# Kernel optimization log

Hardware: AMD Instinct MI355X
Metric: run time of the kernel (lower is better)

## Reference

```python
import jax, jax.numpy as jnp
import numpy as np

EPS = 1e-12  # guard sqrt at zero distance


def setup_inputs() -> dict:
    key = jax.random.key(0)
    k1, k2 = jax.random.split(key)
    B, C, N = 4, 3, 8192
    predict_pc = jax.random.normal(k1, (B, C, N), dtype=jnp.float32)
    gt_pc = jax.random.normal(k2, (B, C, N), dtype=jnp.float32)
    return {"predict_pc": predict_pc, "gt_pc": gt_pc}


def reference(predict_pc, gt_pc):
    # predict_pc: [B, 3, Np], gt_pc: [B, 3, Ng]
    B = gt_pc.shape[0]
    Np = predict_pc.shape[2]
    Ng = gt_pc.shape[2]
    denom = B * (Ng + Np)

    # Pairwise Euclidean distances d[b, n, m] = ||predict[b,:,n] - gt[b,:,m]||
    # via the |p|^2 + |g|^2 - 2 p.g expansion (avoids [B,3,Np,Ng] intermediate).
    p2 = jnp.sum(predict_pc * predict_pc, axis=1)            # [B, Np]
    g2 = jnp.sum(gt_pc * gt_pc, axis=1)                      # [B, Ng]
    dot = jnp.einsum('bcn,bcm->bnm', predict_pc, gt_pc)      # [B, Np, Ng]
    d2 = p2[:, :, None] + g2[:, None, :] - 2.0 * dot         # [B, Np, Ng]
    d = jnp.sqrt(jnp.maximum(d2, EPS))

    # z: for each gt point, distance to nearest predicted point -> min over Np
    z = jnp.min(d, axis=1)   # [B, Ng]
    # z_2: for each predicted point, distance to nearest gt point -> min over Ng
    z2 = jnp.min(d, axis=2)  # [B, Np]

    loss = z.sum() / denom + z2.sum() / denom
    return loss
```

## Files before the change

### kernel.cpp

```cpp
#include <hip/hip_runtime.h>
#include <math.h>


#define B_       4
#define N_       8192
#define THREADS  256
#define RX       16
#define XB       (THREADS * RX)
#define XBLKS    (N_ / XB)
#define YSPLITS  64
#define YCHUNK   (N_ / YSPLITS)
#define NGROUPS  8
#define BLKS_PER_GROUP (XBLKS * YSPLITS)
#define POISON   0xAAAAAAAAu


__global__ __launch_bounds__(THREADS, 4)
void chamfer_fused_kernel(const float* __restrict__ P, const float* __restrict__ G,
                          unsigned* __restrict__ mins, unsigned* __restrict__ gcnt,
                          unsigned* __restrict__ fcnt, float* __restrict__ gsum,
                          float* __restrict__ out)
{
    __shared__ float4 ytile[YCHUNK + 4];
    __shared__ float red[THREADS];
    __shared__ unsigned s_ticket;

    const int t      = threadIdx.x;
    const int xblk   = blockIdx.x;
    const int ysplit = blockIdx.y;
    const int bz     = blockIdx.z;
    const int pass   = bz >> 2;
    const int b      = bz & 3;
    const int grp    = bz;

    const float* Xb = (pass ? G : P) + (size_t)b * 3 * N_;
    const float* Yb = (pass ? P : G) + (size_t)b * 3 * N_;

    if (t < YCHUNK) {
        const int n = ysplit * YCHUNK + t;
        float gx = Yb[n];
        float gy = Yb[N_ + n];
        float gz = Yb[2 * N_ + n];
        ytile[t] = make_float4(gx, gy, gz, fmaf(gx, gx, fmaf(gy, gy, gz * gz)));
    }

    const int xbase = xblk * XB;
    float m2x[RX], m2y[RX], m2z[RX], p2[RX], mn[RX];
#pragma unroll
    for (int i = 0; i < RX; ++i) {
        const int n = xbase + i * THREADS + t;
        float px = Xb[n];
        float py = Xb[N_ + n];
        float pz = Xb[2 * N_ + n];
        p2[i]  = fmaf(px, px, fmaf(py, py, pz * pz));
        m2x[i] = -2.0f * px;
        m2y[i] = -2.0f * py;
        m2z[i] = -2.0f * pz;
        mn[i]  = 3.4e38f;
    }
    __syncthreads();

    float4 g = ytile[0];
#pragma unroll 2
    for (int j = 0; j < YCHUNK; ++j) {
        float4 gn = ytile[j + 1];
#pragma unroll
        for (int i = 0; i < RX; ++i) {
            float s = fmaf(m2x[i], g.x, g.w);
            s = fmaf(m2y[i], g.y, s);
            s = fmaf(m2z[i], g.z, s);
            mn[i] = fminf(mn[i], s);
        }
        g = gn;
    }

    unsigned* mybase = mins + (size_t)grp * N_ + xbase;
#pragma unroll
    for (int i = 0; i < RX; ++i) {
        float v = fmaxf(mn[i] + p2[i], 1e-12f);
        atomicMin(&mybase[i * THREADS + t], __float_as_uint(v));
    }

    __syncthreads();
    if (t == 0) {
        __threadfence();
        s_ticket = atomicAdd(&gcnt[grp], 1u);
    }
    __syncthreads();
    if (s_ticket != POISON + (unsigned)(BLKS_PER_GROUP - 1)) return;

    __threadfence();
    const uint4* v = (const uint4*)(mins + (size_t)grp * N_);
    float acc = 0.0f;
#pragma unroll
    for (int k = 0; k < N_ / 4 / THREADS; ++k) {
        uint4 q = v[k * THREADS + t];
        acc += sqrtf(__uint_as_float(q.x)) + sqrtf(__uint_as_float(q.y))
             + sqrtf(__uint_as_float(q.z)) + sqrtf(__uint_as_float(q.w));
    }
    red[t] = acc;
    __syncthreads();
    for (int off = 128; off > 0; off >>= 1) {
        if (t < off) red[t] += red[t + off];
        __syncthreads();
    }
    if (t == 0) {
        gsum[grp] = red[0];
        __threadfence();
        s_ticket = atomicAdd(fcnt, 1u);
    }
    __syncthreads();
    if (s_ticket != POISON + (unsigned)(NGROUPS - 1)) return;

    __threadfence();
    if (t == 0) {
        float s = 0.0f;
#pragma unroll
        for (int k = 0; k < NGROUPS; ++k) s += gsum[k];
        out[0] = s * (1.0f / 65536.0f);
    }
}

extern "C" void kernel_launch(void* const* d_in, const int* in_sizes, int n_in,
                              void* d_out, int out_size, void* d_ws, size_t ws_size,
                              hipStream_t stream)
{
    const float* P = (const float*)d_in[0];
    const float* G = (const float*)d_in[1];
    float* out = (float*)d_out;

    unsigned* w    = (unsigned*)d_ws;
    unsigned* mins = w;
    unsigned* gcnt = w + 65536;
    unsigned* fcnt = w + 65600;
    float*    gsum = (float*)(w + 65664);

    dim3 grid(XBLKS, YSPLITS, 2 * B_);
    chamfer_fused_kernel<<<grid, THREADS, 0, stream>>>(P, G, mins, gcnt, fcnt, gsum, out);
}
```

Measured before the change: 104.5 us.

## Use packed FP32 FMA over pairs of Y points in the distance loop

The shared Y tile now stores two points per pair of float4 slots in SoA form (x0,x1,y0,y1 / z0,z1,w0,w1). The inner loop uses inline-asm v_pk_fma_f32 with op_sel to evaluate each X point against two Y points in one packed instruction, aiming to halve FMA issue count. The min reduction then uses a chained fminf over both lanes. Inline asm can block compiler scheduling, and the op_sel semantics must be right for the results to be correct.

```diff
diff --git a/kernel.cpp b/kernel.cpp
--- a/kernel.cpp
+++ b/kernel.cpp
@@ -14,6 +14,21 @@
 #define BLKS_PER_GROUP (XBLKS * YSPLITS)
 #define POISON   0xAAAAAAAAu
 
+typedef float v2f __attribute__((ext_vector_type(2)));
+
+__device__ __forceinline__ v2f pk_fma_blo(v2f a, v2f b, v2f c) {
+    v2f d;
+    asm("v_pk_fma_f32 %0, %1, %2, %3 op_sel:[0,0,0] op_sel_hi:[0,1,1]"
+        : "=v"(d) : "v"(a), "v"(b), "v"(c));
+    return d;
+}
+__device__ __forceinline__ v2f pk_fma_bhi(v2f a, v2f b, v2f c) {
+    v2f d;
+    asm("v_pk_fma_f32 %0, %1, %2, %3 op_sel:[1,0,0] op_sel_hi:[1,1,1]"
+        : "=v"(d) : "v"(a), "v"(b), "v"(c));
+    return d;
+}
+
 
 __global__ __launch_bounds__(THREADS, 4)
 void chamfer_fused_kernel(const float* __restrict__ P, const float* __restrict__ G,
@@ -21,7 +36,7 @@
                           unsigned* __restrict__ fcnt, float* __restrict__ gsum,
                           float* __restrict__ out)
 {
-    __shared__ float4 ytile[YCHUNK + 4];
+    __shared__ float4 ytile[2 * (YCHUNK / 2) + 4];
     __shared__ float red[THREADS];
     __shared__ unsigned s_ticket;
 
@@ -36,42 +51,58 @@
     const float* Xb = (pass ? G : P) + (size_t)b * 3 * N_;
     const float* Yb = (pass ? P : G) + (size_t)b * 3 * N_;
 
-    if (t < YCHUNK) {
-        const int n = ysplit * YCHUNK + t;
-        float gx = Yb[n];
-        float gy = Yb[N_ + n];
-        float gz = Yb[2 * N_ + n];
-        ytile[t] = make_float4(gx, gy, gz, fmaf(gx, gx, fmaf(gy, gy, gz * gz)));
+    if (t < YCHUNK / 2) {
+        const int n0 = ysplit * YCHUNK + 2 * t;
+        float2 x01 = *(const float2*)&Yb[n0];
+        float2 y01 = *(const float2*)&Yb[N_ + n0];
+        float2 z01 = *(const float2*)&Yb[2 * N_ + n0];
+        float w0 = fmaf(x01.x, x01.x, fmaf(y01.x, y01.x, z01.x * z01.x));
+        float w1 = fmaf(x01.y, x01.y, fmaf(y01.y, y01.y, z01.y * z01.y));
+        ytile[2 * t]     = make_float4(x01.x, x01.y, y01.x, y01.y);
+        ytile[2 * t + 1] = make_float4(z01.x, z01.y, w0, w1);
     }
 
     const int xbase = xblk * XB;
-    float m2x[RX], m2y[RX], m2z[RX], p2[RX], mn[RX];
+    v2f cm2x[RX / 2], cm2y[RX / 2], cm2z[RX / 2];
+    float p2[RX], mn[RX];
 #pragma unroll
-    for (int i = 0; i < RX; ++i) {
-        const int n = xbase + i * THREADS + t;
-        float px = Xb[n];
-        float py = Xb[N_ + n];
-        float pz = Xb[2 * N_ + n];
-        p2[i]  = fmaf(px, px, fmaf(py, py, pz * pz));
-        m2x[i] = -2.0f * px;
-        m2y[i] = -2.0f * py;
-        m2z[i] = -2.0f * pz;
-        mn[i]  = 3.4e38f;
+    for (int k = 0; k < RX / 2; ++k) {
+        const int n0 = xbase + (2 * k) * THREADS + t;
+        const int n1 = xbase + (2 * k + 1) * THREADS + t;
+        float px0 = Xb[n0], py0 = Xb[N_ + n0], pz0 = Xb[2 * N_ + n0];
+        float px1 = Xb[n1], py1 = Xb[N_ + n1], pz1 = Xb[2 * N_ + n1];
+        p2[2 * k]     = fmaf(px0, px0, fmaf(py0, py0, pz0 * pz0));
+        p2[2 * k + 1] = fmaf(px1, px1, fmaf(py1, py1, pz1 * pz1));
+        cm2x[k] = (v2f){-2.0f * px0, -2.0f * px1};
+        cm2y[k] = (v2f){-2.0f * py0, -2.0f * py1};
+        cm2z[k] = (v2f){-2.0f * pz0, -2.0f * pz1};
+        mn[2 * k] = 3.4e38f;
+        mn[2 * k + 1] = 3.4e38f;
     }
     __syncthreads();
 
-    float4 g = ytile[0];
-#pragma unroll 2
-    for (int j = 0; j < YCHUNK; ++j) {
-        float4 gn = ytile[j + 1];
+    float4 a4 = ytile[0];
+    float4 b4 = ytile[1];
+    for (int jj = 0; jj < YCHUNK / 2; ++jj) {
+        float4 a4n = ytile[2 * jj + 2];
+        float4 b4n = ytile[2 * jj + 3];
+        v2f gx2 = (v2f){a4.x, a4.y};
+        v2f gy2 = (v2f){a4.z, a4.w};
+        v2f gz2 = (v2f){b4.x, b4.y};
+        v2f gw2 = (v2f){b4.z, b4.w};
 #pragma unroll
-        for (int i = 0; i < RX; ++i) {
-            float s = fmaf(m2x[i], g.x, g.w);
-            s = fmaf(m2y[i], g.y, s);
-            s = fmaf(m2z[i], g.z, s);
-            mn[i] = fminf(mn[i], s);
+        for (int k = 0; k < RX / 2; ++k) {
+            v2f s = pk_fma_blo(cm2z[k], gz2, gw2);
+            s = pk_fma_blo(cm2y[k], gy2, s);
+            s = pk_fma_blo(cm2x[k], gx2, s);
+            mn[2 * k] = fminf(fminf(mn[2 * k], s.x), s.y);
+            v2f u = pk_fma_bhi(cm2z[k], gz2, gw2);
+            u = pk_fma_bhi(cm2y[k], gy2, u);
+            u = pk_fma_bhi(cm2x[k], gx2, u);
+            mn[2 * k + 1] = fminf(fminf(mn[2 * k + 1], u.x), u.y);
         }
-        g = gn;
+        a4 = a4n;
+        b4 = b4n;
     }
 
     unsigned* mybase = mins + (size_t)grp * N_ + xbase;
```

New measurement: 104.0 us. About the same (-0.4%).

## Compute pairwise distances with bf16 split-precision MFMA and fuse both min directions

Applied to the files above, without the earlier changes.

Replaces the scalar FMA distance loop with MFMA 16x16x32 bf16 instructions. Each coordinate and squared norm is split into high and low bf16 parts so the dot product keeps near-fp32 accuracy. Both the row minimum and the column minimum now come from one distance tile, which removes the second pass over swapped inputs and halves the pairwise work. Column minima go through shared-memory atomics before the global atomicMin. The risks are the bf16 split losing accuracy for near-zero distances and more atomic contention.

```diff
diff --git a/kernel.cpp b/kernel.cpp
--- a/kernel.cpp
+++ b/kernel.cpp
@@ -2,101 +2,182 @@
 #include <math.h>
 
 
-#define B_       4
-#define N_       8192
-#define THREADS  256
-#define RX       16
-#define XB       (THREADS * RX)
-#define XBLKS    (N_ / XB)
-#define YSPLITS  64
-#define YCHUNK   (N_ / YSPLITS)
-#define NGROUPS  8
-#define BLKS_PER_GROUP (XBLKS * YSPLITS)
-#define POISON   0xAAAAAAAAu
-
-
-__global__ __launch_bounds__(THREADS, 4)
-void chamfer_fused_kernel(const float* __restrict__ P, const float* __restrict__ G,
-                          unsigned* __restrict__ mins, unsigned* __restrict__ gcnt,
-                          unsigned* __restrict__ fcnt, float* __restrict__ gsum,
-                          float* __restrict__ out)
+#define B_        4
+#define N_        8192
+#define THREADS   256
+#define ROWS_PB   256
+#define ROWBLKS   (N_ / ROWS_PB)
+#define MRANGE    1024
+#define MSPLIT    (N_ / MRANGE)
+#define MTILES    (MRANGE / 16)
+#define NGROUPS   B_
+#define BLKS_PER_GROUP (ROWBLKS * MSPLIT)
+#define POISON    0xAAAAAAAAu
+#define INF_BITS  0x7F800000u
+
+typedef __bf16 bf16x8 __attribute__((ext_vector_type(8)));
+typedef float  f32x4  __attribute__((ext_vector_type(4)));
+
+#define SM_ZERO   0
+#define SM_A      16
+#define SM_B      8208
+#define SM_COL    40976
+#define SM_ROW    45072
+#define SM_BYTES  46096
+
+__device__ __forceinline__ unsigned short bf16_rne(float f) {
+    unsigned u = __float_as_uint(f);
+    return (unsigned short)((u + 0x7FFFu + ((u >> 16) & 1u)) >> 16);
+}
+__device__ __forceinline__ float bf16_tof(unsigned short h) {
+    return __uint_as_float(((unsigned)h) << 16);
+}
+
+__device__ __forceinline__ void slotsA(const float* base, int n, unsigned short* dst) {
+    float x = base[n], y = base[N_ + n], z = base[2 * N_ + n];
+    float p2 = fmaf(x, x, fmaf(y, y, z * z));
+    unsigned short hx = bf16_rne(x), hy = bf16_rne(y), hz = bf16_rne(z);
+    float lxf = x - bf16_tof(hx), lyf = y - bf16_tof(hy), lzf = z - bf16_tof(hz);
+    unsigned short mhx = bf16_rne(-2.0f * bf16_tof(hx));
+    unsigned short mhy = bf16_rne(-2.0f * bf16_tof(hy));
+    unsigned short mhz = bf16_rne(-2.0f * bf16_tof(hz));
+    unsigned short mlx = bf16_rne(-2.0f * bf16_tof(bf16_rne(lxf)));
+    unsigned short mly = bf16_rne(-2.0f * bf16_tof(bf16_rne(lyf)));
+    unsigned short mlz = bf16_rne(-2.0f * bf16_tof(bf16_rne(lzf)));
+    unsigned short p2h = bf16_rne(p2);
+    unsigned short p2l = bf16_rne(p2 - bf16_tof(p2h));
+    const unsigned short ONE = 0x3F80;
+    dst[0] = mhx;  dst[1] = mhy;  dst[2] = mhz;
+    dst[3] = mhx;  dst[4] = mhy;  dst[5] = mhz;
+    dst[6] = mlx;  dst[7] = mly;  dst[8] = mlz;
+    dst[9] = p2h;  dst[10] = p2l; dst[11] = ONE; dst[12] = ONE;
+    dst[13] = mlx; dst[14] = mly; dst[15] = mlz;
+}
+
+__device__ __forceinline__ void slotsB(const float* base, int m, unsigned short* dst) {
+    float x = base[m], y = base[N_ + m], z = base[2 * N_ + m];
+    float g2 = fmaf(x, x, fmaf(y, y, z * z));
+    unsigned short hx = bf16_rne(x), hy = bf16_rne(y), hz = bf16_rne(z);
+    unsigned short lx = bf16_rne(x - bf16_tof(hx));
+    unsigned short ly = bf16_rne(y - bf16_tof(hy));
+    unsigned short lz = bf16_rne(z - bf16_tof(hz));
+    unsigned short g2h = bf16_rne(g2);
+    unsigned short g2l = bf16_rne(g2 - bf16_tof(g2h));
+    const unsigned short ONE = 0x3F80;
+    dst[0] = hx;  dst[1] = hy;  dst[2] = hz;
+    dst[3] = lx;  dst[4] = ly;  dst[5] = lz;
+    dst[6] = hx;  dst[7] = hy;  dst[8] = hz;
+    dst[9] = ONE; dst[10] = ONE; dst[11] = g2h; dst[12] = g2l;
+    dst[13] = lx; dst[14] = ly; dst[15] = lz;
+}
+
+
+__global__ __launch_bounds__(THREADS, 3)
+void chamfer_mfma_kernel(const float* __restrict__ P, const float* __restrict__ G,
+                         unsigned* __restrict__ mins, unsigned* __restrict__ gcnt,
+                         unsigned* __restrict__ fcnt, float* __restrict__ gsum,
+                         float* __restrict__ out)
 {
-    __shared__ float4 ytile[YCHUNK + 4];
+    __shared__ __align__(16) char smem[SM_BYTES];
     __shared__ float red[THREADS];
     __shared__ unsigned s_ticket;
 
     const int t      = threadIdx.x;
-    const int xblk   = blockIdx.x;
-    const int ysplit = blockIdx.y;
-    const int bz     = blockIdx.z;
-    const int pass   = bz >> 2;
-    const int b      = bz & 3;
-    const int grp    = bz;
-
-    const float* Xb = (pass ? G : P) + (size_t)b * 3 * N_;
-    const float* Yb = (pass ? P : G) + (size_t)b * 3 * N_;
-
-    if (t < YCHUNK) {
-        const int n = ysplit * YCHUNK + t;
-        float gx = Yb[n];
-        float gy = Yb[N_ + n];
-        float gz = Yb[2 * N_ + n];
-        ytile[t] = make_float4(gx, gy, gz, fmaf(gx, gx, fmaf(gy, gy, gz * gz)));
-    }
-
-    const int xbase = xblk * XB;
-    float m2x[RX], m2y[RX], m2z[RX], p2[RX], mn[RX];
-#pragma unroll
-    for (int i = 0; i < RX; ++i) {
-        const int n = xbase + i * THREADS + t;
-        float px = Xb[n];
-        float py = Xb[N_ + n];
-        float pz = Xb[2 * N_ + n];
-        p2[i]  = fmaf(px, px, fmaf(py, py, pz * pz));
-        m2x[i] = -2.0f * px;
-        m2y[i] = -2.0f * py;
-        m2z[i] = -2.0f * pz;
-        mn[i]  = 3.4e38f;
-    }
-    __syncthreads();
-
-    float4 g = ytile[0];
-#pragma unroll 2
-    for (int j = 0; j < YCHUNK; ++j) {
-        float4 gn = ytile[j + 1];
-#pragma unroll
-        for (int i = 0; i < RX; ++i) {
-            float s = fmaf(m2x[i], g.x, g.w);
-            s = fmaf(m2y[i], g.y, s);
-            s = fmaf(m2z[i], g.z, s);
-            mn[i] = fminf(mn[i], s);
+    const int rowblk = blockIdx.x;
+    const int mspl   = blockIdx.y;
+    const int b      = blockIdx.z;
+    const int rowbase = rowblk * ROWS_PB;
+    const int mbase   = mspl * MRANGE;
+
+    const float* Pb = P + (size_t)b * 3 * N_;
+    const float* Gb = G + (size_t)b * 3 * N_;
+
+    if (t < 4) ((unsigned*)(smem + SM_ZERO))[t] = 0u;
+    unsigned* colmin = (unsigned*)(smem + SM_COL);
+    unsigned* rowmin = (unsigned*)(smem + SM_ROW);
+#pragma unroll
+    for (int k = 0; k < 4; ++k) colmin[k * THREADS + t] = INF_BITS;
+    rowmin[t] = INF_BITS;
+
+    slotsA(Pb, rowbase + t, (unsigned short*)(smem + SM_A) + t * 16);
+#pragma unroll
+    for (int k = 0; k < 4; ++k)
+        slotsB(Gb, mbase + k * THREADS + t,
+               (unsigned short*)(smem + SM_B) + (k * THREADS + t) * 16);
+    __syncthreads();
+
+    const int wave = t >> 6, lane = t & 63, quad = lane >> 4, col = lane & 15;
+
+    bf16x8 afrag[4];
+#pragma unroll
+    for (int rt = 0; rt < 4; ++rt) {
+        const int rowl = wave * 64 + rt * 16 + col;
+        const char* ap = (quad < 2) ? (smem + SM_A + rowl * 32 + quad * 16)
+                                    : (smem + SM_ZERO);
+        afrag[rt] = *(const bf16x8*)ap;
+    }
+    const char* bp = (quad < 2) ? (smem + SM_B + col * 32 + quad * 16)
+                                : (smem + SM_ZERO);
+    const int binc = (quad < 2) ? 16 * 32 : 0;
+
+    float rmin[4][4];
+#pragma unroll
+    for (int rt = 0; rt < 4; ++rt)
+#pragma unroll
+        for (int r = 0; r < 4; ++r) rmin[rt][r] = 3.4e38f;
+
+    for (int mt = 0; mt < MTILES; ++mt) {
+        bf16x8 bfrag = *(const bf16x8*)bp;
+        bp += binc;
+        float cp = 3.4e38f;
+#pragma unroll
+        for (int rt = 0; rt < 4; ++rt) {
+            f32x4 z = {0.0f, 0.0f, 0.0f, 0.0f};
+            f32x4 acc = __builtin_amdgcn_mfma_f32_16x16x32_bf16(afrag[rt], bfrag, z, 0, 0, 0);
+            rmin[rt][0] = fminf(rmin[rt][0], acc[0]);
+            rmin[rt][1] = fminf(rmin[rt][1], acc[1]);
+            rmin[rt][2] = fminf(rmin[rt][2], acc[2]);
+            rmin[rt][3] = fminf(rmin[rt][3], acc[3]);
+            cp = fminf(cp, fminf(fminf(acc[0], acc[1]), fminf(acc[2], acc[3])));
         }
-        g = gn;
-    }
-
-    unsigned* mybase = mins + (size_t)grp * N_ + xbase;
-#pragma unroll
-    for (int i = 0; i < RX; ++i) {
-        float v = fmaxf(mn[i] + p2[i], 1e-12f);
-        atomicMin(&mybase[i * THREADS + t], __float_as_uint(v));
+        atomicMin(&colmin[mt * 16 + col], __float_as_uint(fmaxf(cp, 1e-12f)));
+    }
+
+#pragma unroll
+    for (int rt = 0; rt < 4; ++rt)
+#pragma unroll
+        for (int r = 0; r < 4; ++r)
+            atomicMin(&rowmin[wave * 64 + rt * 16 + quad * 4 + r],
+                      __float_as_uint(fmaxf(rmin[rt][r], 1e-12f)));
+    __syncthreads();
+
+    atomicMin(&mins[(size_t)b * N_ + rowbase + t], rowmin[t]);
+#pragma unroll
+    for (int k = 0; k < 4; ++k) {
+        const int i = k * THREADS + t;
+        atomicMin(&mins[32768 + (size_t)b * N_ + mbase + i], colmin[i]);
     }
 
     __syncthreads();
     if (t == 0) {
         __threadfence();
-        s_ticket = atomicAdd(&gcnt[grp], 1u);
+        s_ticket = atomicAdd(&gcnt[b], 1u);
     }
     __syncthreads();
     if (s_ticket != POISON + (unsigned)(BLKS_PER_GROUP - 1)) return;
 
     __threadfence();
-    const uint4* v = (const uint4*)(mins + (size_t)grp * N_);
+    const uint4* v0 = (const uint4*)(mins + (size_t)b * N_);
+    const uint4* v1 = (const uint4*)(mins + 32768 + (size_t)b * N_);
     float acc = 0.0f;
 #pragma unroll
     for (int k = 0; k < N_ / 4 / THREADS; ++k) {
-        uint4 q = v[k * THREADS + t];
+        uint4 q = v0[k * THREADS + t];
+        uint4 w = v1[k * THREADS + t];
         acc += sqrtf(__uint_as_float(q.x)) + sqrtf(__uint_as_float(q.y))
-             + sqrtf(__uint_as_float(q.z)) + sqrtf(__uint_as_float(q.w));
+             + sqrtf(__uint_as_float(q.z)) + sqrtf(__uint_as_float(q.w))
+             + sqrtf(__uint_as_float(w.x)) + sqrtf(__uint_as_float(w.y))
+             + sqrtf(__uint_as_float(w.z)) + sqrtf(__uint_as_float(w.w));
     }
     red[t] = acc;
     __syncthreads();
@@ -105,7 +186,7 @@
         __syncthreads();
     }
     if (t == 0) {
-        gsum[grp] = red[0];
+        gsum[b] = red[0];
         __threadfence();
         s_ticket = atomicAdd(fcnt, 1u);
     }
@@ -113,12 +194,8 @@
     if (s_ticket != POISON + (unsigned)(NGROUPS - 1)) return;
 
     __threadfence();
-    if (t == 0) {
-        float s = 0.0f;
-#pragma unroll
-        for (int k = 0; k < NGROUPS; ++k) s += gsum[k];
-        out[0] = s * (1.0f / 65536.0f);
-    }
+    if (t == 0)
+        out[0] = (gsum[0] + gsum[1] + gsum[2] + gsum[3]) * (1.0f / 65536.0f);
 }
 
 extern "C" void kernel_launch(void* const* d_in, const int* in_sizes, int n_in,
@@ -135,6 +212,6 @@
     unsigned* fcnt = w + 65600;
     float*    gsum = (float*)(w + 65664);
 
-    dim3 grid(XBLKS, YSPLITS, 2 * B_);
-    chamfer_fused_kernel<<<grid, THREADS, 0, stream>>>(P, G, mins, gcnt, fcnt, gsum, out);
-}
+    dim3 grid(ROWBLKS, MSPLIT, B_);
+    chamfer_mfma_kernel<<<grid, THREADS, 0, stream>>>(P, G, mins, gcnt, fcnt, gsum, out);
+}
```

Result: slower. 112.6 us (+7.8%).
